# Performance work log

Measured on AMD Instinct MI355X. Metric: run time of the kernel, lower is better.

The kernel has to match this reference:

```python
import jax, jax.numpy as jnp
import numpy as np

SMOOTH_STEP_PARAM = 1.0  # = 1/gamma in the TEL paper
DEPTH = 6


def smooth_step(x):
    # TEL smooth-step: 0 for u<=-1/2, 1 for u>=1/2, cubic -2u^3+1.5u+0.5 inside.
    u = SMOOTH_STEP_PARAM * x
    inner = (-2.0 * u + 1.5) * u * u + (u + 0.5) * 0.0 + (-2.0 * u ** 3 + 1.5 * u + 0.5)
    # use single clean expression for the cubic
    cubic = -2.0 * u ** 3 + 1.5 * u + 0.5
    return jnp.where(u <= -0.5, 0.0, jnp.where(u >= 0.5, 1.0, cubic))


def setup_inputs() -> dict:
    key = jax.random.key(0)
    k1, k2, k3 = jax.random.split(key, 3)
    B, D, T, O = 32768, 1024, 8, 128
    num_leaves = 2 ** DEPTH
    x = jax.random.normal(k1, (B, D), dtype=jnp.float32)
    # RandomUniform(-0.01, 0.01) initializers in the original layer
    node_weights = jax.random.uniform(k2, (T, D, num_leaves - 1), dtype=jnp.float32,
                                      minval=-0.01, maxval=0.01)
    leaf_weights = jax.random.uniform(k3, (T, O, num_leaves), dtype=jnp.float32,
                                      minval=-0.01, maxval=0.01)
    return {"x": x, "node_weights": node_weights, "leaf_weights": leaf_weights}


def reference(x, node_weights, leaf_weights):
    B = x.shape[0]
    T = node_weights.shape[0]
    # routing probabilities at every internal node (BFS order): [B, T, 2^depth-1]
    s = smooth_step(jnp.einsum('bd,tdi->bti', x, node_weights))
    # accumulate leaf reach probabilities level by level (left child gets s)
    mu = jnp.ones((B, T, 1), dtype=x.dtype)
    start = 0
    for level in range(DEPTH):
        width = 2 ** level
        s_lvl = s[:, :, start:start + width]           # [B, T, width]
        mu = jnp.stack([mu * s_lvl, mu * (1.0 - s_lvl)], axis=-1)
        mu = mu.reshape(B, T, 2 * width)
        start += width
    # weighted sum of leaf vectors, summed over trees (sum_outputs=True)
    return jnp.einsum('btl,tol->bo', mu, leaf_weights)
```

## Files before the change

### kernel.cpp

```cpp
#include <hip/hip_runtime.h>
#include <hip/hip_bf16.h>
#include <stdint.h>

#define KDIM 1024
#define TSTR 72
#define RSTR 576

typedef __attribute__((ext_vector_type(4))) float f32x4;
typedef __attribute__((ext_vector_type(8))) short bf16x8;

#define WS_LB_OFF ((size_t)1 << 20)

__device__ __forceinline__ unsigned short f2bf_rne(float f) {
    unsigned u = __float_as_uint(f);
    u = (u + 0x7fffu + ((u >> 16) & 1u)) >> 16;
    return (unsigned short)u;
}

__device__ __forceinline__ unsigned int pack2_bf16(float a, float b) {
    __hip_bfloat162 h = __float22bfloat162_rn(make_float2(a, b));
    union { __hip_bfloat162 h; unsigned int u; } cv;
    cv.h = h;
    return cv.u;
}

__device__ __forceinline__ float gs_get(const uint4* q, int i) {
    uint4 v = q[i >> 3];
    int c = (i >> 1) & 3;
    unsigned w = (c == 0) ? v.x : (c == 1) ? v.y : (c == 2) ? v.z : v.w;
    return __uint_as_float((i & 1) ? (w & 0xffff0000u) : (w << 16));
}

__global__ void prep_w(const float* __restrict__ nw, unsigned short* __restrict__ wb) {
    int idx = blockIdx.x * 256 + threadIdx.x;
    int kl = idx & 31;
    int n  = (idx >> 5) & 511;
    int ks = idx >> 14;
    int cp = kl >> 3, e = kl & 7;
    int kchunk = cp ^ (n & 3);
    int d = ks * 32 + kchunk * 8 + e;
    int t = n >> 6, i = n & 63;
    float v = (i < 63) ? nw[(t * KDIM + d) * 63 + i] : 0.0f;
    wb[idx] = f2bf_rne(v);
}

__global__ void prep_l(const float* __restrict__ lw, unsigned short* __restrict__ lb) {
    int idx = blockIdx.x * 256 + threadIdx.x;
    int kk = idx & 31;
    int o  = (idx >> 5) & 127;
    int kq = idx >> 12;
    int c = kq * 32 + kk;
    int t = c >> 6, l = c & 63;
    lb[idx] = f2bf_rne(lw[(t * 128 + o) * 64 + l]);
}

__launch_bounds__(256, 2)
__global__ void fused(const float* __restrict__ x, const unsigned short* __restrict__ wb,
                      const unsigned short* __restrict__ lb, float* __restrict__ out) {
    __shared__ __align__(16) unsigned short xs[32 * 40];
    __shared__ __align__(16) unsigned short wl[512 * 32];
    __shared__ __align__(16) unsigned short st[32 * RSTR];

    const int tid  = threadIdx.x;
    const int wave = tid >> 6, lane = tid & 63;
    const int quad = lane >> 4, l16 = lane & 15;
    const int mb   = blockIdx.x;

    f32x4 acc[8][2];
    const f32x4 z4 = {0.f, 0.f, 0.f, 0.f};
    #pragma unroll
    for (int a = 0; a < 8; ++a) { acc[a][0] = z4; acc[a][1] = z4; }

    const int xrow = tid >> 3, xq8 = tid & 7;
    const float* xg0 = x + (size_t)(mb * 32 + xrow) * KDIM + xq8 * 4;

    for (int ks = 0; ks < 32; ++ks) {
        __threadfence_block();
        __syncthreads();
        const unsigned short* wks = wb + (size_t)ks * (512 * 32);
        #pragma unroll
        for (int h = 0; h < 2; ++h) {
            uint4 wv[4];
            #pragma unroll
            for (int it = 0; it < 4; ++it)
                wv[it] = *(const uint4*)(wks + (size_t)((h * 4 + it) * 256 + tid) * 8);
            #pragma unroll
            for (int it = 0; it < 4; ++it)
                *(uint4*)&wl[((h * 4 + it) * 256 + tid) * 8] = wv[it];
        }
        {
            float4 f0 = *(const float4*)(xg0 + ks * 32);
            uint2 pk;
            pk.x = pack2_bf16(f0.x, f0.y);
            pk.y = pack2_bf16(f0.z, f0.w);
            *(uint2*)&xs[xrow * 40 + xq8 * 4] = pk;
        }
        __threadfence_block();
        __syncthreads();
        bf16x8 af[8], bfr[2];
        #pragma unroll
        for (int ct = 0; ct < 8; ++ct) {
            int col = wave * 128 + ct * 16 + l16;
            int chunk = quad ^ (col & 3);
            af[ct] = *(const bf16x8*)&wl[col * 32 + chunk * 8];
        }
        #pragma unroll
        for (int rt = 0; rt < 2; ++rt)
            bfr[rt] = *(const bf16x8*)&xs[(rt * 16 + l16) * 40 + quad * 8];
        #pragma unroll
        for (int ct = 0; ct < 8; ++ct)
            #pragma unroll
            for (int rt = 0; rt < 2; ++rt)
                acc[ct][rt] = __builtin_amdgcn_mfma_f32_16x16x32_bf16(af[ct], bfr[rt], acc[ct][rt], 0, 0, 0);
    }

    __threadfence_block();
    __syncthreads();
    #pragma unroll
    for (int rt2 = 0; rt2 < 2; ++rt2) {
        int row = rt2 * 16 + l16;
        #pragma unroll
        for (int ct = 0; ct < 8; ++ct) {
            int colb = wave * 128 + ct * 16 + quad * 4;
            f32x4 a = acc[ct][rt2];
            float s0[4];
            #pragma unroll
            for (int j = 0; j < 4; ++j) {
                float u = a[j];
                u = fminf(fmaxf(u, -0.5f), 0.5f);
                s0[j] = u * (1.5f - 2.0f * u * u) + 0.5f;
            }
            uint2 pk;
            pk.x = pack2_bf16(s0[0], s0[1]);
            pk.y = pack2_bf16(s0[2], s0[3]);
            *(uint2*)&st[row * RSTR + (colb >> 6) * TSTR + (colb & 63)] = pk;
        }
    }
    __syncthreads();
    {
        int r = tid >> 3, t = tid & 7;
        unsigned short* base = &st[r * RSTR + t * TSTR];
        uint4 q[8];
        #pragma unroll
        for (int c = 0; c < 8; ++c) q[c] = *(const uint4*)(base + c * 8);
        float mu[32];
        mu[0] = 1.0f;
        int start = 0;
        #pragma unroll
        for (int lvl = 0; lvl < 5; ++lvl) {
            int width = 1 << lvl;
            #pragma unroll
            for (int j = width - 1; j >= 0; --j) {
                float m = mu[j], s_ = gs_get(q, start + j);
                mu[2 * j + 1] = m * (1.0f - s_);
                mu[2 * j]     = m * s_;
            }
            start += width;
        }
        #pragma unroll
        for (int c = 0; c < 8; ++c) {
            unsigned pk2[4];
            #pragma unroll
            for (int e = 0; e < 4; ++e) {
                int j = c * 4 + e;
                float m = mu[j], s_ = gs_get(q, 31 + j);
                pk2[e] = pack2_bf16(m * s_, m * (1.0f - s_));
            }
            uint4 v; v.x = pk2[0]; v.y = pk2[1]; v.z = pk2[2]; v.w = pk2[3];
            *(uint4*)(base + c * 8) = v;
        }
    }
    __syncthreads();
    {
        int rtile = wave & 1, ob = (wave >> 1) * 64;
        f32x4 a2[4];
        a2[0] = z4; a2[1] = z4; a2[2] = z4; a2[3] = z4;
        #pragma unroll
        for (int kq = 0; kq < 16; ++kq) {
            int c0 = kq * 32 + quad * 8;
            bf16x8 bmu = *(const bf16x8*)&st[(rtile * 16 + l16) * RSTR + (c0 >> 6) * TSTR + (c0 & 63)];
            #pragma unroll
            for (int ct = 0; ct < 4; ++ct) {
                int o = ob + ct * 16 + l16;
                bf16x8 alf = *(const bf16x8*)(lb + (size_t)(kq * 128 + o) * 32 + quad * 8);
                a2[ct] = __builtin_amdgcn_mfma_f32_16x16x32_bf16(alf, bmu, a2[ct], 0, 0, 0);
            }
        }
        #pragma unroll
        for (int ct = 0; ct < 4; ++ct) {
            int rowg = mb * 32 + rtile * 16 + l16;
            int og = ob + ct * 16 + quad * 4;
            *(f32x4*)(out + (size_t)rowg * 128 + og) = a2[ct];
        }
    }
}

extern "C" void kernel_launch(void* const* d_in, const int* in_sizes, int n_in,
                              void* d_out, int out_size, void* d_ws, size_t ws_size,
                              hipStream_t stream) {
    const float* x  = (const float*)d_in[0];
    const float* nw = (const float*)d_in[1];
    const float* lw = (const float*)d_in[2];
    float* out = (float*)d_out;

    unsigned short* wb = (unsigned short*)d_ws;
    unsigned short* lb = (unsigned short*)((char*)d_ws + WS_LB_OFF);

    prep_w<<<2048, 256, 0, stream>>>(nw, wb);
    prep_l<<<256, 256, 0, stream>>>(lw, lb);
    fused<<<1024, 256, 0, stream>>>(x, wb, lb, out);
}
```

Baseline: 273.4 us.

## Load weight fragments directly from global memory, double-buffer x tile in LDS

The GEMM stage no longer stages the 512x32 weight tile through shared memory. Each wave reads its MFMA A-fragments straight from global memory (L2-resident), which removes an LDS round-trip and one barrier per k-step. The x tile is now double-buffered so only a single __syncthreads is needed per iteration. The weight prep drops the XOR swizzle, the stats row stride is padded to 584, and launch bounds ask for 3 blocks per CU. The trade-off is more global/L2 traffic, since every block re-reads all the weights without any LDS reuse across waves, plus possible register pressure at the higher occupancy target.

```diff
diff --git a/kernel.cpp b/kernel.cpp
--- a/kernel.cpp
+++ b/kernel.cpp
@@ -4,7 +4,7 @@
 
 #define KDIM 1024
 #define TSTR 72
-#define RSTR 576
+#define RSTR 584
 
 typedef __attribute__((ext_vector_type(4))) float f32x4;
 typedef __attribute__((ext_vector_type(8))) short bf16x8;
@@ -36,9 +36,7 @@
     int kl = idx & 31;
     int n  = (idx >> 5) & 511;
     int ks = idx >> 14;
-    int cp = kl >> 3, e = kl & 7;
-    int kchunk = cp ^ (n & 3);
-    int d = ks * 32 + kchunk * 8 + e;
+    int d = ks * 32 + kl;
     int t = n >> 6, i = n & 63;
     float v = (i < 63) ? nw[(t * KDIM + d) * 63 + i] : 0.0f;
     wb[idx] = f2bf_rne(v);
@@ -54,11 +52,10 @@
     lb[idx] = f2bf_rne(lw[(t * 128 + o) * 64 + l]);
 }
 
-__launch_bounds__(256, 2)
+__launch_bounds__(256, 3)
 __global__ void fused(const float* __restrict__ x, const unsigned short* __restrict__ wb,
                       const unsigned short* __restrict__ lb, float* __restrict__ out) {
-    __shared__ __align__(16) unsigned short xs[32 * 40];
-    __shared__ __align__(16) unsigned short wl[512 * 32];
+    __shared__ __align__(16) unsigned short xs[2][32 * 40];
     __shared__ __align__(16) unsigned short st[32 * RSTR];
 
     const int tid  = threadIdx.x;
@@ -73,48 +70,37 @@
 
     const int xrow = tid >> 3, xq8 = tid & 7;
     const float* xg0 = x + (size_t)(mb * 32 + xrow) * KDIM + xq8 * 4;
+    const unsigned short* wfrag = wb + (size_t)(wave * 128 + l16) * 32 + quad * 8;
 
     for (int ks = 0; ks < 32; ++ks) {
-        __threadfence_block();
-        __syncthreads();
-        const unsigned short* wks = wb + (size_t)ks * (512 * 32);
-        #pragma unroll
-        for (int h = 0; h < 2; ++h) {
-            uint4 wv[4];
-            #pragma unroll
-            for (int it = 0; it < 4; ++it)
-                wv[it] = *(const uint4*)(wks + (size_t)((h * 4 + it) * 256 + tid) * 8);
-            #pragma unroll
-            for (int it = 0; it < 4; ++it)
-                *(uint4*)&wl[((h * 4 + it) * 256 + tid) * 8] = wv[it];
-        }
         {
             float4 f0 = *(const float4*)(xg0 + ks * 32);
             uint2 pk;
             pk.x = pack2_bf16(f0.x, f0.y);
             pk.y = pack2_bf16(f0.z, f0.w);
-            *(uint2*)&xs[xrow * 40 + xq8 * 4] = pk;
+            *(uint2*)&xs[ks & 1][xrow * 40 + xq8 * 4] = pk;
         }
-        __threadfence_block();
         __syncthreads();
-        bf16x8 af[8], bfr[2];
-        #pragma unroll
-        for (int ct = 0; ct < 8; ++ct) {
-            int col = wave * 128 + ct * 16 + l16;
-            int chunk = quad ^ (col & 3);
-            af[ct] = *(const bf16x8*)&wl[col * 32 + chunk * 8];
-        }
+        bf16x8 bfr[2];
         #pragma unroll
         for (int rt = 0; rt < 2; ++rt)
-            bfr[rt] = *(const bf16x8*)&xs[(rt * 16 + l16) * 40 + quad * 8];
+            bfr[rt] = *(const bf16x8*)&xs[ks & 1][(rt * 16 + l16) * 40 + quad * 8];
+        const unsigned short* wks = wfrag + (size_t)ks * (512 * 32);
         #pragma unroll
-        for (int ct = 0; ct < 8; ++ct)
+        for (int h = 0; h < 2; ++h) {
+            bf16x8 af[4];
             #pragma unroll
-            for (int rt = 0; rt < 2; ++rt)
-                acc[ct][rt] = __builtin_amdgcn_mfma_f32_16x16x32_bf16(af[ct], bfr[rt], acc[ct][rt], 0, 0, 0);
+            for (int c4 = 0; c4 < 4; ++c4)
+                af[c4] = *(const bf16x8*)(wks + (h * 4 + c4) * (16 * 32));
+            #pragma unroll
+            for (int c4 = 0; c4 < 4; ++c4)
+                #pragma unroll
+                for (int rt = 0; rt < 2; ++rt)
+                    acc[h * 4 + c4][rt] =
+                        __builtin_amdgcn_mfma_f32_16x16x32_bf16(af[c4], bfr[rt], acc[h * 4 + c4][rt], 0, 0, 0);
+        }
     }
 
-    __threadfence_block();
     __syncthreads();
     #pragma unroll
     for (int rt2 = 0; rt2 < 2; ++rt2) {
```

After: 307.6 us. 1.13x slower.
